# Kernel tuning notes

Measured on AMD Instinct MI355X. Metric: run time of the kernel, lower is better.

## Reference

```python
import jax, jax.numpy as jnp
import numpy as np

B, N, D_NODE, D_EDGE, D_GRAPH = 2, 1024, 128, 16, 128
MID, OUT = 64, 128


def _linear_params(key, fan_in, fan_out):
    # haiku Linear default: truncated-normal(stddev=1/sqrt(fan_in)) weight, zero bias
    w = jax.random.normal(key, (fan_in, fan_out), dtype=jnp.float32) / np.sqrt(fan_in)
    b = jnp.zeros((fan_out,), dtype=jnp.float32)
    return w, b


def setup_inputs() -> dict:
    key = jax.random.key(0)
    ks = jax.random.split(key, 12)
    features = jax.random.normal(ks[0], (B, N, D_NODE), dtype=jnp.float32)
    e_features = jax.random.normal(ks[1], (B, N, N, D_EDGE), dtype=jnp.float32)
    g_features = jax.random.normal(ks[2], (B, D_GRAPH), dtype=jnp.float32)
    adj = jax.random.randint(ks[3], (B, N, N), 0, 2).astype(jnp.float32)
    # ensure self-loops so every row has at least one valid neighbor
    adj = jnp.maximum(adj, jnp.eye(N, dtype=jnp.float32)[None])
    Wm, bm = _linear_params(ks[4], D_NODE, OUT)
    Wskip, bskip = _linear_params(ks[5], D_NODE, OUT)
    W1, b1 = _linear_params(ks[6], D_NODE, MID)
    W2, b2 = _linear_params(ks[7], D_NODE, MID)
    We, be = _linear_params(ks[8], D_EDGE, MID)
    Wg, bg = _linear_params(ks[9], D_GRAPH, MID)
    Wa, ba = _linear_params(ks[10], MID, 1)
    return dict(features=features, e_features=e_features, g_features=g_features,
                adj=adj, Wm=Wm, bm=bm, Wskip=Wskip, bskip=bskip,
                W1=W1, b1=b1, W2=W2, b2=b2, We=We, be=be, Wg=Wg, bg=bg,
                Wa=Wa, ba=ba)


def reference(features, e_features, g_features, adj,
              Wm, bm, Wskip, bskip, W1, b1, W2, b2, We, be, Wg, bg, Wa, ba):
    # bias mask: 0 where edge exists, -1e9 where not
    bias_mat = (adj - 1.0) * 1e9  # (b,n,n)

    values = features @ Wm + bm          # (b,n,out)
    pre_att_1 = features @ W1 + b1       # (b,n,mid) -> per-target j
    pre_att_2 = features @ W2 + b2       # (b,n,mid) -> per-source i
    pre_att_e = e_features @ We + be     # (b,n,n,mid)
    pre_att_g = g_features @ Wg + bg     # (b,mid)

    # pre_att[b,i,j] = p1[b,j] + p2[b,i] + pe[b,i,j] + pg[b]
    pre_att = (pre_att_1[:, None, :, :] + pre_att_2[:, :, None, :]
               + pre_att_e + pre_att_g[:, None, None, :])  # (b,n,n,mid)

    logits = jnp.squeeze(jax.nn.leaky_relu(pre_att) @ Wa + ba, axis=-1)  # (b,n,n)
    coefs = jax.nn.softmax(logits + bias_mat, axis=-1)                   # (b,n,n)

    ret = jnp.matmul(coefs, values)       # (b,n,out)
    ret = ret + (features @ Wskip + bskip)  # residual
    return jax.nn.relu(ret)               # activation=relu
```

## Files before the change

### kernel.cpp

```cpp
#include <hip/hip_runtime.h>
#include <hip/hip_bf16.h>
#include <cstdint>

#define B_   2
#define N_   1024
#define DN_  128
#define DE_  16
#define DG_  128
#define MID_ 64
#define OUT_ 128
#define TI_  2
#define PR_ROWS 4

typedef short bf16x8 __attribute__((ext_vector_type(8)));
typedef float f32x4  __attribute__((ext_vector_type(4)));

__device__ inline short f2bf(float f) {
    union { float f; unsigned u; } v; v.f = f;
    unsigned r = v.u + 0x7FFFu + ((v.u >> 16) & 1u);
    return (short)(unsigned short)(r >> 16);
}

__device__ inline unsigned pk2(float lo, float hi) {
    union { __hip_bfloat162 h; unsigned u; } p;
    p.h = __float22bfloat162_rn(make_float2(lo, hi));
    return p.u;
}

__global__ void __launch_bounds__(384) prep_all(
    const float* __restrict__ features, const float* __restrict__ g_features,
    const float* __restrict__ Wm, const float* __restrict__ bm,
    const float* __restrict__ Wskip, const float* __restrict__ bskip,
    const float* __restrict__ W1, const float* __restrict__ b1,
    const float* __restrict__ W2, const float* __restrict__ b2,
    const float* __restrict__ We, const float* __restrict__ be,
    const float* __restrict__ Wg, const float* __restrict__ bg,
    float* __restrict__ values, float* __restrict__ skipo,
    float* __restrict__ P1x, float* __restrict__ p2,
    float* __restrict__ pg, short* __restrict__ We_frag)
{
    const int t   = threadIdx.x;
    const int blk = blockIdx.x;

    if (blk == 512) {
        for (int e = t; e < 4 * 64 * 8; e += 384) {
            const int c    = e >> 9;
            const int lane = (e >> 3) & 63;
            const int j    = e & 7;
            const int quad = lane >> 4, s = lane & 15;
            short v = 0;
            if (quad < 2) v = f2bf(We[(quad * 8 + j) * MID_ + c * 16 + s]);
            We_frag[e] = v;
        }
        return;
    }
    if (blk == 513) {
        if (t < MID_) {
            float a0 = bg[t], a1 = bg[t];
            for (int k = 0; k < DG_; ++k) {
                const float w = Wg[k * MID_ + t];
                a0 += g_features[k] * w;
                a1 += g_features[DG_ + k] * w;
            }
            pg[t] = a0; pg[MID_ + t] = a1;
        }
        return;
    }

    const int r0 = blk * PR_ROWS;
    __shared__ float feat[PR_ROWS][DN_];
    for (int idx = t; idx < PR_ROWS * DN_; idx += 384)
        feat[idx >> 7][idx & 127] = features[(size_t)r0 * DN_ + idx];
    __syncthreads();

    const float* W; int c, stride; float base; float* outp; int ostride;
    if (t < 128) {
        W = Wm;    c = t;       stride = OUT_; base = bm[c];
        outp = values + (size_t)r0 * OUT_ + c; ostride = OUT_;
    } else if (t < 256) {
        W = Wskip; c = t - 128; stride = OUT_; base = bskip[c];
        outp = skipo + (size_t)r0 * OUT_ + c;  ostride = OUT_;
    } else if (t < 320) {
        W = W1;    c = t - 256; stride = MID_; base = b1[c] + be[c];
        outp = P1x + (size_t)r0 * MID_ + c;    ostride = MID_;
    } else {
        W = W2;    c = t - 320; stride = MID_; base = b2[c];
        outp = p2 + (size_t)r0 * MID_ + c;     ostride = MID_;
    }

    float acc[PR_ROWS] = {};
    for (int k = 0; k < DN_; ++k) {
        const float w = W[k * stride + c];
        #pragma unroll
        for (int q = 0; q < PR_ROWS; ++q) acc[q] += feat[q][k] * w;
    }
    #pragma unroll
    for (int q = 0; q < PR_ROWS; ++q) outp[q * ostride] = acc[q] + base;
}

__global__ void __launch_bounds__(256) k_logits(
    const float* __restrict__ e_features, const short* __restrict__ We_frag,
    const float* __restrict__ Wa, const float* __restrict__ P1x,
    const float* __restrict__ p2, const float* __restrict__ pg,
    float* __restrict__ lg)
{
    const int t    = threadIdx.x;
    const int wv   = t >> 6;
    const int l    = t & 63;
    const int quad = l >> 4;
    const int s    = l & 15;
    const int r    = blockIdx.x;
    const int jb   = r & 1;
    const int ri   = r >> 1;
    const int b    = ri >> 9;
    const int i0   = (ri & 511) * TI_;

    bf16x8 bfr[4];
    float4 wa4[4];
    f32x4  p2l[TI_][4];
    #pragma unroll
    for (int c = 0; c < 4; ++c) {
        bfr[c] = *(const bf16x8*)&We_frag[(c * 64 + l) * 8];
        wa4[c] = *(const float4*)&Wa[c * 16 + quad * 4];
        const float4 pg4 = *(const float4*)&pg[b * MID_ + c * 16 + quad * 4];
        #pragma unroll
        for (int ii = 0; ii < TI_; ++ii) {
            const float4 p4 = *(const float4*)&p2[((size_t)(b * N_ + i0 + ii)) * MID_ + c * 16 + quad * 4];
            p2l[ii][c][0] = p4.x + pg4.x;
            p2l[ii][c][1] = p4.y + pg4.y;
            p2l[ii][c][2] = p4.z + pg4.z;
            p2l[ii][c][3] = p4.w + pg4.w;
        }
    }
    const size_t erow0 = (size_t)(b * N_ + i0) * N_;
    const int jt0 = jb * 32;

    float4 eB[3][TI_][2];
    float  bb[2][4][4];

    auto loadE = [&](float4 (&dst)[TI_][2], int tile) {
        if (quad < 2) {
            #pragma unroll
            for (int ii = 0; ii < TI_; ++ii) {
                const float* ep = &e_features[(erow0 + (size_t)ii * N_ + (size_t)tile * 16 + s) * DE_ + quad * 8];
                dst[ii][0] = *(const float4*)ep;
                dst[ii][1] = *(const float4*)(ep + 4);
            }
        }
    };
    auto loadB = [&](float (&dst)[4][4], int tile) {
        const float* pb = &P1x[(size_t)(b * N_ + tile * 16 + s) * MID_ + quad * 4];
        #pragma unroll
        for (int c = 0; c < 4; ++c) {
            const float4 v = *(const float4*)(pb + c * 16);
            dst[c][0] = v.x; dst[c][1] = v.y; dst[c][2] = v.z; dst[c][3] = v.w;
        }
    };

    loadE(eB[0], jt0 + wv);
    loadE(eB[1], jt0 + wv + 4);
    loadE(eB[2], jt0 + wv + 8);
    loadB(bb[0], jt0 + wv);

    #pragma unroll
    for (int it = 0; it < 8; ++it) {
        const int tile = jt0 + wv + it * 4;
        const int j0   = tile * 16;

        unsigned af[TI_][4];
        #pragma unroll
        for (int ii = 0; ii < TI_; ++ii) {
            if (quad < 2) {
                af[ii][0] = pk2(eB[it % 3][ii][0].x, eB[it % 3][ii][0].y);
                af[ii][1] = pk2(eB[it % 3][ii][0].z, eB[it % 3][ii][0].w);
                af[ii][2] = pk2(eB[it % 3][ii][1].x, eB[it % 3][ii][1].y);
                af[ii][3] = pk2(eB[it % 3][ii][1].z, eB[it % 3][ii][1].w);
            } else {
                af[ii][0] = af[ii][1] = af[ii][2] = af[ii][3] = 0u;
            }
        }
        if (it < 5) loadE(eB[it % 3], tile + 12);
        if (it < 7) loadB(bb[(it + 1) & 1], tile + 4);

        #pragma unroll
        for (int ii = 0; ii < TI_; ++ii) {
            union { unsigned u[4]; bf16x8 v; } a;
            a.u[0] = af[ii][0]; a.u[1] = af[ii][1];
            a.u[2] = af[ii][2]; a.u[3] = af[ii][3];
            f32x4 acc[4];
            #pragma unroll
            for (int c = 0; c < 4; ++c)
                acc[c] = __builtin_amdgcn_mfma_f32_16x16x32_bf16(bfr[c], a.v, p2l[ii][c], 0, 0, 0);
            float part = 0.f;
            #pragma unroll
            for (int c = 0; c < 4; ++c) {
                #pragma unroll
                for (int rr = 0; rr < 4; ++rr) {
                    float x = acc[c][rr] + bb[it & 1][c][rr];
                    x = fmaxf(x, 0.01f * x);
                    part += x * (c == 0 ? (rr == 0 ? wa4[0].x : rr == 1 ? wa4[0].y : rr == 2 ? wa4[0].z : wa4[0].w)
                               : c == 1 ? (rr == 0 ? wa4[1].x : rr == 1 ? wa4[1].y : rr == 2 ? wa4[1].z : wa4[1].w)
                               : c == 2 ? (rr == 0 ? wa4[2].x : rr == 1 ? wa4[2].y : rr == 2 ? wa4[2].z : wa4[2].w)
                                        : (rr == 0 ? wa4[3].x : rr == 1 ? wa4[3].y : rr == 2 ? wa4[3].z : wa4[3].w));
                }
            }
            part += __shfl_xor(part, 16);
            part += __shfl_xor(part, 32);
            if (l < 16)
                lg[((size_t)(b * N_ + i0 + ii)) * N_ + j0 + l] = part;
        }
    }
}

__global__ void __launch_bounds__(256) k_attn(
    const float* __restrict__ lg, const float* __restrict__ adj,
    const float* __restrict__ values, const float* __restrict__ skipo,
    float* __restrict__ out)
{
    const int t  = threadIdx.x;
    const int wv = t >> 6;
    const int l  = t & 63;
    const int r  = blockIdx.x;
    const int b  = (r >> 2) & 1;
    const int i0 = (((r >> 3) << 2) | (r & 3)) * TI_;

    __shared__ float lgP[TI_][N_];
    __shared__ float redv[4][16][20];
    __shared__ float sinv[TI_];
    __shared__ float pmax[4];
    __shared__ float psum[4];

    {
        const int rw = wv & 1, h = wv >> 1;
        const int c0 = h * 512 + l * 4;
        const float* lrow = &lg[(size_t)(b * N_ + i0 + rw) * N_];
        const size_t arb  = (size_t)(b * N_ + i0 + rw) * N_;
        float4 lv[2], av[2];
        #pragma unroll
        for (int q = 0; q < 2; ++q) {
            lv[q] = *(const float4*)&lrow[c0 + 256 * q];
            av[q] = *(const float4*)&adj[arb + c0 + 256 * q];
        }
        const float NEG = -3.4e38f;
        float m = NEG;
        #pragma unroll
        for (int q = 0; q < 2; ++q) {
            m = fmaxf(m, av[q].x > 0.f ? lv[q].x : NEG);
            m = fmaxf(m, av[q].y > 0.f ? lv[q].y : NEG);
            m = fmaxf(m, av[q].z > 0.f ? lv[q].z : NEG);
            m = fmaxf(m, av[q].w > 0.f ? lv[q].w : NEG);
        }
        #pragma unroll
        for (int o = 1; o < 64; o <<= 1) m = fmaxf(m, __shfl_xor(m, o));
        if (l == 0) pmax[wv] = m;
        __syncthreads();
        m = fmaxf(pmax[rw], pmax[2 + rw]);
        float sum = 0.f;
        #pragma unroll
        for (int q = 0; q < 2; ++q) {
            float4 e4;
            e4.x = av[q].x > 0.f ? __expf(lv[q].x - m) : 0.f;
            e4.y = av[q].y > 0.f ? __expf(lv[q].y - m) : 0.f;
            e4.z = av[q].z > 0.f ? __expf(lv[q].z - m) : 0.f;
            e4.w = av[q].w > 0.f ? __expf(lv[q].w - m) : 0.f;
            *(float4*)&lgP[rw][c0 + 256 * q] = e4;
            sum += (e4.x + e4.y) + (e4.z + e4.w);
        }
        #pragma unroll
        for (int o = 1; o < 64; o <<= 1) sum += __shfl_xor(sum, o);
        if (l == 0) psum[wv] = sum;
        __syncthreads();
        if (t < TI_) sinv[t] = 1.0f / (psum[t] + psum[t + 2]);
    }

    const int cg = l & 15, jp = l >> 4, ch0 = cg * 8;
    float acc[TI_][8] = {};
    const float* vb = values + (size_t)b * N_ * OUT_ + ch0;
    for (int k = 0; k < 64; ++k) {
        const int j = wv * 4 + jp + k * 16;
        float cw[TI_];
        #pragma unroll
        for (int ii = 0; ii < TI_; ++ii) cw[ii] = lgP[ii][j];
        const float* vp = vb + (size_t)j * OUT_;
        const float4 v0 = *(const float4*)vp;
        const float4 v1 = *(const float4*)(vp + 4);
        const float vv[8] = {v0.x, v0.y, v0.z, v0.w, v1.x, v1.y, v1.z, v1.w};
        #pragma unroll
        for (int ii = 0; ii < TI_; ++ii)
            #pragma unroll
            for (int kk = 0; kk < 8; ++kk)
                acc[ii][kk] += cw[ii] * vv[kk];
    }
    #pragma unroll
    for (int ii = 0; ii < TI_; ++ii)
        #pragma unroll
        for (int kk = 0; kk < 8; ++kk) {
            acc[ii][kk] += __shfl_xor(acc[ii][kk], 16);
            acc[ii][kk] += __shfl_xor(acc[ii][kk], 32);
        }
    if (l < 16) {
        #pragma unroll
        for (int ii = 0; ii < TI_; ++ii)
            #pragma unroll
            for (int q = 0; q < 2; ++q) {
                float4 w4 = make_float4(acc[ii][q * 4], acc[ii][q * 4 + 1],
                                        acc[ii][q * 4 + 2], acc[ii][q * 4 + 3]);
                *(float4*)&redv[wv][l][ii * 8 + q * 4] = w4;
            }
    }
    __syncthreads();
    {
        const int ch = t & 127, g = ch >> 3, kk = ch & 7;
        const int ii = t >> 7;
        float sum = redv[0][g][ii * 8 + kk];
        #pragma unroll
        for (int w = 1; w < 4; ++w) sum += redv[w][g][ii * 8 + kk];
        const size_t ob = ((size_t)(b * N_ + i0 + ii)) * OUT_ + ch;
        out[ob] = fmaxf(sum * sinv[ii] + skipo[ob], 0.f);
    }
}

extern "C" void kernel_launch(void* const* d_in, const int* in_sizes, int n_in,
                              void* d_out, int out_size, void* d_ws, size_t ws_size,
                              hipStream_t stream) {
    const float* features   = (const float*)d_in[0];
    const float* e_features = (const float*)d_in[1];
    const float* g_features = (const float*)d_in[2];
    const float* adj        = (const float*)d_in[3];
    const float* Wm    = (const float*)d_in[4];
    const float* bm    = (const float*)d_in[5];
    const float* Wskip = (const float*)d_in[6];
    const float* bskip = (const float*)d_in[7];
    const float* W1    = (const float*)d_in[8];
    const float* b1    = (const float*)d_in[9];
    const float* W2    = (const float*)d_in[10];
    const float* b2    = (const float*)d_in[11];
    const float* We    = (const float*)d_in[12];
    const float* be    = (const float*)d_in[13];
    const float* Wg    = (const float*)d_in[14];
    const float* bg    = (const float*)d_in[15];
    const float* Wa    = (const float*)d_in[16];
    float* out = (float*)d_out;

    float* ws      = (float*)d_ws;
    float* values  = ws;
    float* skipo   = ws + 262144;
    float* P1x     = ws + 524288;
    float* p2      = ws + 655360;
    float* pg      = ws + 786432;
    short* We_frag = (short*)(ws + 786560);
    float* lg      = ws + 787584;

    prep_all<<<B_ * N_ / PR_ROWS + 2, 384, 0, stream>>>(
        features, g_features, Wm, bm, Wskip, bskip, W1, b1, W2, b2,
        We, be, Wg, bg, values, skipo, P1x, p2, pg, We_frag);
    k_logits<<<B_ * N_ / TI_ * 2, 256, 0, stream>>>(
        e_features, We_frag, Wa, P1x, p2, pg, lg);
    k_attn<<<B_ * N_ / TI_, 256, 0, stream>>>(
        lg, adj, values, skipo, out);
}
```

Baseline: 298.6 us.

## Fuse logits and attention kernels, keeping logits in shared memory

Merges the logits kernel into the attention kernel so each block computes its two rows of logits over all 1024 columns directly into shared memory, then runs softmax and aggregation. This removes the global write and re-read of the full logits matrix and one kernel launch. In exchange, the grid shrinks to half as many blocks (1024 instead of 2048), each doing twice the logits work. The e_features prefetch depth drops from triple to double buffering, which may expose more memory latency.

```diff
diff --git a/kernel.cpp b/kernel.cpp
--- a/kernel.cpp
+++ b/kernel.cpp
@@ -98,11 +98,12 @@
     for (int q = 0; q < PR_ROWS; ++q) outp[q * ostride] = acc[q] + base;
 }
 
-__global__ void __launch_bounds__(256) k_logits(
-    const float* __restrict__ e_features, const short* __restrict__ We_frag,
-    const float* __restrict__ Wa, const float* __restrict__ P1x,
-    const float* __restrict__ p2, const float* __restrict__ pg,
-    float* __restrict__ lg)
+__global__ void __launch_bounds__(256) gat_main(
+    const float* __restrict__ e_features, const float* __restrict__ adj,
+    const short* __restrict__ We_frag, const float* __restrict__ Wa,
+    const float* __restrict__ values, const float* __restrict__ skipo,
+    const float* __restrict__ P1x, const float* __restrict__ p2,
+    const float* __restrict__ pg, float* __restrict__ out)
 {
     const int t    = threadIdx.x;
     const int wv   = t >> 6;
@@ -110,10 +111,14 @@
     const int quad = l >> 4;
     const int s    = l & 15;
     const int r    = blockIdx.x;
-    const int jb   = r & 1;
-    const int ri   = r >> 1;
-    const int b    = ri >> 9;
-    const int i0   = (ri & 511) * TI_;
+    const int b    = (r >> 2) & 1;
+    const int i0   = (((r >> 3) << 2) | (r & 3)) * TI_;
+
+    __shared__ float lgP[TI_][N_];
+    __shared__ float redv[4][16][20];
+    __shared__ float sinv[TI_];
+    __shared__ float pmax[4];
+    __shared__ float psum[4];
 
     bf16x8 bfr[4];
     float4 wa4[4];
@@ -133,54 +138,53 @@
         }
     }
     const size_t erow0 = (size_t)(b * N_ + i0) * N_;
-    const int jt0 = jb * 32;
-
-    float4 eB[3][TI_][2];
+
+    float4 eA[2][TI_][2];
     float  bb[2][4][4];
 
-    auto loadE = [&](float4 (&dst)[TI_][2], int tile) {
+    auto loadE = [&](int buf, int tile) {
         if (quad < 2) {
             #pragma unroll
             for (int ii = 0; ii < TI_; ++ii) {
                 const float* ep = &e_features[(erow0 + (size_t)ii * N_ + (size_t)tile * 16 + s) * DE_ + quad * 8];
-                dst[ii][0] = *(const float4*)ep;
-                dst[ii][1] = *(const float4*)(ep + 4);
+                eA[buf][ii][0] = *(const float4*)ep;
+                eA[buf][ii][1] = *(const float4*)(ep + 4);
             }
         }
     };
-    auto loadB = [&](float (&dst)[4][4], int tile) {
+    auto loadB = [&](int buf, int tile) {
         const float* pb = &P1x[(size_t)(b * N_ + tile * 16 + s) * MID_ + quad * 4];
         #pragma unroll
         for (int c = 0; c < 4; ++c) {
             const float4 v = *(const float4*)(pb + c * 16);
-            dst[c][0] = v.x; dst[c][1] = v.y; dst[c][2] = v.z; dst[c][3] = v.w;
+            bb[buf][c][0] = v.x; bb[buf][c][1] = v.y;
+            bb[buf][c][2] = v.z; bb[buf][c][3] = v.w;
         }
     };
 
-    loadE(eB[0], jt0 + wv);
-    loadE(eB[1], jt0 + wv + 4);
-    loadE(eB[2], jt0 + wv + 8);
-    loadB(bb[0], jt0 + wv);
+    loadE(0, wv);
+    loadE(1, wv + 4);
+    loadB(0, wv);
 
     #pragma unroll
-    for (int it = 0; it < 8; ++it) {
-        const int tile = jt0 + wv + it * 4;
+    for (int it = 0; it < 16; ++it) {
+        const int tile = wv + it * 4;
         const int j0   = tile * 16;
 
         unsigned af[TI_][4];
         #pragma unroll
         for (int ii = 0; ii < TI_; ++ii) {
             if (quad < 2) {
-                af[ii][0] = pk2(eB[it % 3][ii][0].x, eB[it % 3][ii][0].y);
-                af[ii][1] = pk2(eB[it % 3][ii][0].z, eB[it % 3][ii][0].w);
-                af[ii][2] = pk2(eB[it % 3][ii][1].x, eB[it % 3][ii][1].y);
-                af[ii][3] = pk2(eB[it % 3][ii][1].z, eB[it % 3][ii][1].w);
+                af[ii][0] = pk2(eA[it & 1][ii][0].x, eA[it & 1][ii][0].y);
+                af[ii][1] = pk2(eA[it & 1][ii][0].z, eA[it & 1][ii][0].w);
+                af[ii][2] = pk2(eA[it & 1][ii][1].x, eA[it & 1][ii][1].y);
+                af[ii][3] = pk2(eA[it & 1][ii][1].z, eA[it & 1][ii][1].w);
             } else {
                 af[ii][0] = af[ii][1] = af[ii][2] = af[ii][3] = 0u;
             }
         }
-        if (it < 5) loadE(eB[it % 3], tile + 12);
-        if (it < 7) loadB(bb[(it + 1) & 1], tile + 4);
+        if (it < 14) loadE(it & 1, tile + 8);
+        if (it < 15) loadB((it + 1) & 1, tile + 4);
 
         #pragma unroll
         for (int ii = 0; ii < TI_; ++ii) {
@@ -206,39 +210,19 @@
             }
             part += __shfl_xor(part, 16);
             part += __shfl_xor(part, 32);
-            if (l < 16)
-                lg[((size_t)(b * N_ + i0 + ii)) * N_ + j0 + l] = part;
-        }
-    }
-}
-
-__global__ void __launch_bounds__(256) k_attn(
-    const float* __restrict__ lg, const float* __restrict__ adj,
-    const float* __restrict__ values, const float* __restrict__ skipo,
-    float* __restrict__ out)
-{
-    const int t  = threadIdx.x;
-    const int wv = t >> 6;
-    const int l  = t & 63;
-    const int r  = blockIdx.x;
-    const int b  = (r >> 2) & 1;
-    const int i0 = (((r >> 3) << 2) | (r & 3)) * TI_;
-
-    __shared__ float lgP[TI_][N_];
-    __shared__ float redv[4][16][20];
-    __shared__ float sinv[TI_];
-    __shared__ float pmax[4];
-    __shared__ float psum[4];
+            if (l < 16) lgP[ii][j0 + l] = part;
+        }
+    }
+    __syncthreads();
 
     {
         const int rw = wv & 1, h = wv >> 1;
         const int c0 = h * 512 + l * 4;
-        const float* lrow = &lg[(size_t)(b * N_ + i0 + rw) * N_];
-        const size_t arb  = (size_t)(b * N_ + i0 + rw) * N_;
+        const size_t arb = (size_t)(b * N_ + i0 + rw) * N_;
         float4 lv[2], av[2];
         #pragma unroll
         for (int q = 0; q < 2; ++q) {
-            lv[q] = *(const float4*)&lrow[c0 + 256 * q];
+            lv[q] = *(const float4*)&lgP[rw][c0 + 256 * q];
             av[q] = *(const float4*)&adj[arb + c0 + 256 * q];
         }
         const float NEG = -3.4e38f;
@@ -349,13 +333,10 @@
     float* p2      = ws + 655360;
     float* pg      = ws + 786432;
     short* We_frag = (short*)(ws + 786560);
-    float* lg      = ws + 787584;
 
     prep_all<<<B_ * N_ / PR_ROWS + 2, 384, 0, stream>>>(
         features, g_features, Wm, bm, Wskip, bskip, W1, b1, W2, b2,
         We, be, Wg, bg, values, skipo, P1x, p2, pg, We_frag);
-    k_logits<<<B_ * N_ / TI_ * 2, 256, 0, stream>>>(
-        e_features, We_frag, Wa, P1x, p2, pg, lg);
-    k_attn<<<B_ * N_ / TI_, 256, 0, stream>>>(
-        lg, adj, values, skipo, out);
-}
+    gat_main<<<B_ * N_ / TI_, 256, 0, stream>>>(
+        e_features, adj, We_frag, Wa, values, skipo, P1x, p2, pg, out);
+}
```

Measured after the change: 284.5 us. -4.7%, faster.
